# Performance work log

Measured on AMD Instinct MI355X. Metric: run time of the kernel, lower is better.

The kernel has to match this reference:

```python
import math
import jax, jax.numpy as jnp
import numpy as np

# Module config (init_kwargs)
GRID = (11, 16, 24)          # (T, H, W) latent grid, T odd so T-1 == 2*(T//2)
POOL = 128                   # pool_size / block size
SPARSITY = 0.9
TXT_LEN = 384                # txt_len, txt_first=False
HEADS, HDIM = 8, 128
FFL = GRID[1] * GRID[2]      # first_frame_len = H*W = 384
SEQ = GRID[0] * FFL + TXT_LEN  # 4608 tokens, 36 blocks of 128


def _rearr(t):
    # rearrange_with_remaining, h%8==0 and w%8==0 path.
    # t: [b, (f h w), n, d] with f = T-1 frames (first frame excluded)
    b, s, n, d = t.shape
    T, H, W = GRID
    fn, hn, wn = T // 2, H // 8, W // 8
    x = t.transpose(0, 2, 1, 3).reshape(b * n, fn, 2, hn, 8, wn, 8, d)
    # 'b (fn fb)(hn hb)(wn wb) d -> b (fn hn wn fb hb wb) d'
    x = x.transpose(0, 1, 3, 5, 2, 4, 6, 7).reshape(b * n, s, d)
    return x.reshape(b, n, s, d).transpose(0, 2, 1, 3)


def _inv_rearr(t):
    b, s, n, d = t.shape
    T, H, W = GRID
    fn, hn, wn = T // 2, H // 8, W // 8
    x = t.transpose(0, 2, 1, 3).reshape(b * n, fn, hn, wn, 2, 8, 8, d)
    x = x.transpose(0, 1, 4, 2, 5, 3, 6, 7).reshape(b * n, s, d)
    return x.reshape(b, n, s, d).transpose(0, 2, 1, 3)


def _avgpool(t):
    # seq divisible by POOL -> mean over each block (tail branch unused)
    b, s, n, d = t.shape
    return t.reshape(b, s // POOL, POOL, n, d).mean(axis=2)


def _forward(q, k, v):
    b, s, n, d = q.shape
    scale = jnp.asarray(d, q.dtype) ** -0.5
    # do_tensor_rearrange_pooling on concatenated qkv (txt_first=False)
    qkv = jnp.concatenate([q, k, v], axis=0)
    f_part = qkv[:, :FFL]
    i_part = qkv[:, FFL:s - TXT_LEN]
    t_part = qkv[:, s - TXT_LEN:]
    qkv2 = jnp.concatenate([_rearr(i_part), f_part, t_part], axis=1)
    pool = _avgpool(qkv2)
    q2, k2, v2 = jnp.split(qkv2, 3, axis=0)
    qp, kp, _ = jnp.split(pool, 3, axis=0)
    # pooled block scores + softmax
    ps = jax.nn.softmax(jnp.einsum('blnd,bsnd->bnls', qp, kp) * scale, axis=-1)
    nb = s // POOL
    keep = math.ceil(nb * (1.0 - SPARSITY))
    thr = jax.lax.top_k(ps, keep)[0][..., -1:]
    mask = ps >= thr                              # [B, n, nb, nb] bool
    prot = (FFL + TXT_LEN + POOL - 1) // POOL
    mask = mask.at[:, :, -prot:, :].set(True)
    mask = mask.at[:, :, :, -prot:].set(True)
    bm = mask[0]                                  # [n, nb, nb] per-head block mask (batch 0, as kernel uses)
    tok = jnp.repeat(jnp.repeat(bm, POOL, axis=1), POOL, axis=2)  # [n, S, S]
    # block-sparse attention == masked dense attention over selected kv blocks
    scores = jnp.einsum('bqnd,bknd->bnqk', q2, k2) * scale
    scores = jnp.where(tok[None], scores, jnp.asarray(-1e30, scores.dtype))
    p = jax.nn.softmax(scores, axis=-1)
    x = jnp.einsum('bnqk,bknd->bqnd', p, v2)
    # do_tensor_inv_rearrange (txt_first=False: concat(f, i, t))
    si = s - TXT_LEN - FFL
    xi = _inv_rearr(x[:, :si])
    xf = x[:, si:si + FFL]
    xt = x[:, si + FFL:]
    return jnp.concatenate([xf, xi, xt], axis=1)


def setup_inputs() -> dict:
    key = jax.random.key(0)
    kq, kk, kv = jax.random.split(key, 3)
    q = jax.random.normal(kq, (1, SEQ, HEADS, HDIM), dtype=jnp.float32)
    k = jax.random.normal(kk, (1, SEQ, HEADS, HDIM), dtype=jnp.float32)
    v = jax.random.normal(kv, (1, SEQ, HEADS, HDIM), dtype=jnp.float32)
    t_b_idx = jnp.arange(2, dtype=jnp.int64 if jax.config.jax_enable_x64 else jnp.int32)
    return {'q': q, 'k': k, 'v': v, 't_b_idx': t_b_idx}


def reference(q, k, v, t_b_idx):
    # t_idx = t_b_idx[0] = 0, skip_timesteps = 0 -> sparse branch (static)
    return _forward(q, k, v)
```

## Files before the change

kernel.cpp:

```cpp
#include <hip/hip_runtime.h>


typedef __attribute__((ext_vector_type(8))) _Float16 half8;
typedef __attribute__((ext_vector_type(4))) _Float16 half4;
typedef __attribute__((ext_vector_type(4))) float float4v;

#define KROW 136
#define VROW 72
#define PPROW 40

__device__ __forceinline__ int orig_pos(int j) {
    if (j >= 3840) return (j < 4224) ? (j - 3840) : j;
    int blk = j >> 7;
    int r   = j & 127;
    int f   = blk / 6;
    int rem = blk - f * 6;
    int b2  = rem / 3;
    int e   = rem - b2 * 3;
    int a   = r >> 6;
    int c   = (r >> 3) & 7;
    int g   = r & 7;
    return 384 + (f * 2 + a) * 384 + (b2 * 8 + c) * 24 + e * 8 + g;
}

__global__ __launch_bounds__(256) void prep_kernel(const float* __restrict__ q,
                                                   const float* __restrict__ k,
                                                   const float* __restrict__ v,
                                                   short* __restrict__ Kc,
                                                   unsigned* __restrict__ Vt32,
                                                   float* __restrict__ qp,
                                                   float* __restrict__ kp) {
    __shared__ short Vs[64 * KROW];
    __shared__ float Rs[8 * 128];
    int bx  = blockIdx.x;
    int tid = threadIdx.x;

    if (bx < 576) {
        int sub = bx & 1;
        int kb  = (bx >> 1) % 36;
        int h   = bx / 72;

        int lr = tid >> 3;
        int ld = (tid & 7) << 2;
#pragma unroll
        for (int pass = 0; pass < 2; ++pass) {
            int lt  = pass * 32 + lr;
            int tok = sub * 64 + lt;
            int op  = orig_pos(kb * 128 + tok);
            const float* kr = k + ((size_t)op * 8 + h) * 128;
            const float* vr = v + ((size_t)op * 8 + h) * 128;
            short* ko = Kc + ((size_t)(h * 36 + kb) * 128 + tok) * KROW;
#pragma unroll
            for (int j = 0; j < 4; ++j) {
                int d = ld + j * 32;
                float4v xk = *reinterpret_cast<const float4v*>(kr + d);
                float4v xv = *reinterpret_cast<const float4v*>(vr + d);
                half4 hk, hv;
#pragma unroll
                for (int i = 0; i < 4; ++i) { hk[i] = (_Float16)xk[i]; hv[i] = (_Float16)xv[i]; }
                *reinterpret_cast<half4*>(ko + d) = hk;
                *reinterpret_cast<half4*>(&Vs[lt * KROW + d]) = hv;
            }
        }
        __syncthreads();

        {
            const unsigned short* Vsu = (const unsigned short*)Vs;
            unsigned* vo = Vt32 + (size_t)((h * 36 + kb) * 2 + sub) * 128 * (VROW / 2);
#pragma unroll
            for (int it = 0; it < 16; ++it) {
                int i   = it * 256 + tid;
                int tw  = i & 31;
                int dim = i >> 5;
                unsigned lo = Vsu[(2 * tw) * KROW + dim];
                unsigned hi = Vsu[(2 * tw + 1) * KROW + dim];
                vo[dim * (VROW / 2) + tw] = (hi << 16) | lo;
            }
        }
    } else {
        int bx2 = bx - 576;
        int sub = bx2 & 1;
        int kb  = (bx2 >> 1) % 36;
        int h   = bx2 / 72;

        const float* arr = sub ? q : k;
        int dq = (tid & 31) << 2;
        int g  = tid >> 5;
        float4v acc = {0.f, 0.f, 0.f, 0.f};
#pragma unroll
        for (int it = 0; it < 16; ++it) {
            int t  = g + it * 8;
            int op = orig_pos(kb * 128 + t);
            float4v x = *reinterpret_cast<const float4v*>(arr + ((size_t)op * 8 + h) * 128 + dq);
            acc[0] += x[0]; acc[1] += x[1]; acc[2] += x[2]; acc[3] += x[3];
        }
#pragma unroll
        for (int i = 0; i < 4; ++i) Rs[g * 128 + dq + i] = acc[i];
        __syncthreads();

        if (tid < 128) {
            float s = 0.f;
#pragma unroll
            for (int g2 = 0; g2 < 8; ++g2) s += Rs[g2 * 128 + tid];
            float* outp = sub ? qp : kp;
            outp[(h * 36 + kb) * 128 + tid] = s * (1.f / 128.f);
        }
    }
}

__global__ __launch_bounds__(256, 3) void flash_kernel(const float* __restrict__ q,
                                                       const short* __restrict__ Kc,
                                                       const short* __restrict__ Vt,
                                                       const float* __restrict__ qp,
                                                       const float* __restrict__ kp,
                                                       float* __restrict__ out,
                                                       float* __restrict__ pO,
                                                       float* __restrict__ pL) {
    __shared__ __align__(16) short Ph[4 * 32 * PPROW];
    __shared__ __align__(16) float Red[2][32 * 132];
    __shared__ int Ls[40];
    __shared__ float Lf[64];

    int t = blockIdx.x;
    int h, qb, half, nkb = 0, kbase = 0, pidx = -1;
    if (t < 288) {
        h = t & 7;
        int rest = t >> 3;
        int qbh = rest / 6, r2 = rest % 6;
        half = r2 / 3;
        int chunk = r2 % 3;
        qb = 30 + qbh; nkb = 12; kbase = chunk * 12; pidx = t;
    } else {
        int t2 = t - 288;
        h = t2 & 7;
        int rest = t2 >> 3;
        qb = rest >> 1; half = rest & 1;
    }

    int tid = threadIdx.x, wave = tid >> 6, lane = tid & 63;
    int m16 = lane & 15, quad = lane >> 4;
    int rh = wave & 1, th = wave >> 1;

    constexpr float kScale = 0.08838834764831845f * 1.4426950408889634f;

    half8 aq[2][4];
#pragma unroll
    for (int rg = 0; rg < 2; ++rg) {
        int qrow_frag = qb * 128 + half * 64 + rh * 32 + rg * 16 + m16;
        const float* qrp = q + ((size_t)orig_pos(qrow_frag) * 8 + h) * 128;
#pragma unroll
        for (int kc = 0; kc < 4; ++kc) {
            float4v x0 = *reinterpret_cast<const float4v*>(qrp + kc * 32 + quad * 8);
            float4v x1 = *reinterpret_cast<const float4v*>(qrp + kc * 32 + quad * 8 + 4);
#pragma unroll
            for (int j = 0; j < 4; ++j) {
                aq[rg][kc][j]     = (_Float16)(x0[j] * kScale);
                aq[rg][kc][4 + j] = (_Float16)(x1[j] * kScale);
            }
        }
    }

    if (pidx < 0 && wave == 0) {
        float s = -1e30f;
        if (lane < 36) {
            const float4v* qv = (const float4v*)(qp + (h * 36 + qb) * 128);
            const float4v* kv = (const float4v*)(kp + (h * 36 + lane) * 128);
            float acc = 0.f;
            for (int i = 0; i < 32; ++i) {
                float4v a = qv[i], b = kv[i];
                acc += a[0] * b[0] + a[1] * b[1] + a[2] * b[2] + a[3] * b[3];
            }
            s = acc;
        }
        float tmp = s;
        float thr = 0.f;
        for (int i = 0; i < 4; ++i) {
            float mx = tmp;
            for (int off = 1; off < 64; off <<= 1) mx = fmaxf(mx, __shfl_xor(mx, off));
            thr = mx;
            unsigned long long bal = __ballot(tmp == mx);
            int low = __ffsll(bal) - 1;
            if (lane == low) tmp = -3e38f;
        }
        bool keep = (lane < 36) && ((s >= thr) || (lane >= 30));
        unsigned long long mk = __ballot(keep);
        if (lane == 0) Ls[0] = __popcll(mk);
        if (keep) {
            int pos = __popcll(mk & ((1ull << lane) - 1ull));
            Ls[1 + pos] = lane;
        }
    }
    __syncthreads();
    if (pidx < 0) nkb = Ls[0];

    float l_r[2][4];
    float4v o[2][8];
#pragma unroll
    for (int rg = 0; rg < 2; ++rg) {
#pragma unroll
        for (int r = 0; r < 4; ++r) l_r[rg][r] = 0.f;
#pragma unroll
        for (int dt = 0; dt < 8; ++dt) { o[rg][dt][0] = 0.f; o[rg][dt][1] = 0.f; o[rg][dt][2] = 0.f; o[rg][dt][3] = 0.f; }
    }

    short* Phw = Ph + wave * (32 * PPROW);

    int kfo = (th * 32 + m16) * KROW + quad * 8;
    int vfo = m16 * VROW + th * 32 + quad * 8;

    int ntile = nkb * 2;
    for (int it = 0; it < ntile; ++it) {
        int kb  = (pidx >= 0) ? (kbase + (it >> 1)) : Ls[1 + (it >> 1)];
        int sub = it & 1;
        const short* gK = Kc + ((size_t)((h * 36 + kb) * 128) + sub * 64) * KROW;
        const short* gV = Vt + (size_t)((h * 36 + kb) * 2 + sub) * 128 * VROW;

        float4v sacc[2][2];
#pragma unroll
        for (int rg = 0; rg < 2; ++rg)
#pragma unroll
            for (int nt = 0; nt < 2; ++nt) { sacc[rg][nt][0] = 0.f; sacc[rg][nt][1] = 0.f; sacc[rg][nt][2] = 0.f; sacc[rg][nt][3] = 0.f; }
#pragma unroll
        for (int nt = 0; nt < 2; ++nt)
#pragma unroll
            for (int kc = 0; kc < 4; ++kc) {
                half8 bk = *reinterpret_cast<const half8*>(gK + kfo + nt * (16 * KROW) + kc * 32);
                sacc[0][nt] = __builtin_amdgcn_mfma_f32_16x16x32_f16(aq[0][kc], bk, sacc[0][nt], 0, 0, 0);
                sacc[1][nt] = __builtin_amdgcn_mfma_f32_16x16x32_f16(aq[1][kc], bk, sacc[1][nt], 0, 0, 0);
            }

#pragma unroll
        for (int rg = 0; rg < 2; ++rg)
#pragma unroll
            for (int r = 0; r < 4; ++r) {
                float p0 = exp2f(sacc[rg][0][r]);
                float p1 = exp2f(sacc[rg][1][r]);
                sacc[rg][0][r] = p0; sacc[rg][1][r] = p1;
                l_r[rg][r] += p0 + p1;
            }

#pragma unroll
        for (int rg = 0; rg < 2; ++rg)
#pragma unroll
            for (int nt = 0; nt < 2; ++nt)
#pragma unroll
                for (int r = 0; r < 4; ++r) {
                    union { _Float16 hf; short s; } cv;
                    cv.hf = (_Float16)sacc[rg][nt][r];
                    Phw[(rg * 16 + quad * 4 + r) * PPROW + nt * 16 + m16] = cv.s;
                }
        half8 ap[2];
#pragma unroll
        for (int rg = 0; rg < 2; ++rg)
            ap[rg] = *reinterpret_cast<const half8*>(&Phw[(rg * 16 + m16) * PPROW + quad * 8]);

#pragma unroll
        for (int dt = 0; dt < 8; ++dt) {
            half8 bv = *reinterpret_cast<const half8*>(gV + vfo + dt * (16 * VROW));
            o[0][dt] = __builtin_amdgcn_mfma_f32_16x16x32_f16(ap[0], bv, o[0][dt], 0, 0, 0);
            o[1][dt] = __builtin_amdgcn_mfma_f32_16x16x32_f16(ap[1], bv, o[1][dt], 0, 0, 0);
        }
    }

#pragma unroll
    for (int rg = 0; rg < 2; ++rg)
#pragma unroll
        for (int r = 0; r < 4; ++r)
            for (int sh = 1; sh < 16; sh <<= 1) l_r[rg][r] += __shfl_xor(l_r[rg][r], sh);

    __syncthreads();
    {
        float* red = &Red[rh][0];
        if (th == 1) {
#pragma unroll
            for (int rg = 0; rg < 2; ++rg) {
#pragma unroll
                for (int dt = 0; dt < 8; ++dt)
#pragma unroll
                    for (int r = 0; r < 4; ++r)
                        red[(rg * 16 + quad * 4 + r) * 132 + dt * 16 + m16] = o[rg][dt][r];
                if (m16 == 0)
#pragma unroll
                    for (int r = 0; r < 4; ++r)
                        Lf[rh * 32 + rg * 16 + quad * 4 + r] = l_r[rg][r];
            }
        }
        __syncthreads();
        if (th == 0) {
#pragma unroll
            for (int rg = 0; rg < 2; ++rg)
#pragma unroll
                for (int dt = 0; dt < 8; ++dt)
#pragma unroll
                    for (int r = 0; r < 4; ++r)
                        o[rg][dt][r] += red[(rg * 16 + quad * 4 + r) * 132 + dt * 16 + m16];

            if (pidx >= 0) {
                float* po = pO + (size_t)pidx * 8192;
#pragma unroll
                for (int rg = 0; rg < 2; ++rg)
#pragma unroll
                    for (int r = 0; r < 4; ++r) {
                        int row = rh * 32 + rg * 16 + quad * 4 + r;
                        float lt2 = l_r[rg][r] + Lf[row];
#pragma unroll
                        for (int dt = 0; dt < 8; ++dt)
                            po[row * 128 + dt * 16 + m16] = o[rg][dt][r];
                        if (m16 == 0) pL[pidx * 64 + row] = lt2;
                    }
            } else {
#pragma unroll
                for (int rg = 0; rg < 2; ++rg)
#pragma unroll
                    for (int r = 0; r < 4; ++r) {
                        int row = rh * 32 + rg * 16 + quad * 4 + r;
                        int qrow = qb * 128 + half * 64 + row;
                        size_t base = ((size_t)orig_pos(qrow) * 8 + h) * 128;
                        float inv = 1.f / (l_r[rg][r] + Lf[row]);
#pragma unroll
                        for (int dt = 0; dt < 8; ++dt)
                            out[base + dt * 16 + m16] = o[rg][dt][r] * inv;
                    }
            }
        }
    }
}

__global__ void combine_kernel(const float* __restrict__ pO, const float* __restrict__ pL,
                               float* __restrict__ out) {
    int gb = blockIdx.x;
    int g  = gb >> 3;
    int rg = gb & 7;
    int h    = g / 12;
    int rem  = g % 12;
    int qbh  = rem >> 1;
    int half = rem & 1;
    int qb   = 30 + qbh;
    int base_t = (qbh * 6 + half * 3) * 8 + h;

    int tid = threadIdx.x;
    int d   = tid & 127;
    int r0  = tid >> 7;
#pragma unroll
    for (int itr = 0; itr < 4; ++itr) {
        int row = rg * 8 + r0 + itr * 2;
        float l = pL[(base_t + 0) * 64 + row] + pL[(base_t + 8) * 64 + row] + pL[(base_t + 16) * 64 + row];
        float acc = pO[(size_t)(base_t + 0) * 8192 + row * 128 + d]
                  + pO[(size_t)(base_t + 8) * 8192 + row * 128 + d]
                  + pO[(size_t)(base_t + 16) * 8192 + row * 128 + d];
        int qrow = qb * 128 + half * 64 + row;
        out[((size_t)orig_pos(qrow) * 8 + h) * 128 + d] = acc / l;
    }
}

extern "C" void kernel_launch(void* const* d_in, const int* in_sizes, int n_in,
                              void* d_out, int out_size, void* d_ws, size_t ws_size,
                              hipStream_t stream) {
    const float* q = (const float*)d_in[0];
    const float* k = (const float*)d_in[1];
    const float* v = (const float*)d_in[2];
    float* out = (float*)d_out;

    char* w = (char*)d_ws;
    short* Kc  = (short*)(w);
    short* Vt  = (short*)(w + 10027008);
    float* qp  = (float*)(w + 20643840);
    float* kp  = (float*)(w + 20791296);
    float* pL  = (float*)(w + 20938752);
    float* pO  = (float*)(w + 21012480);

    prep_kernel<<<dim3(1152), dim3(256), 0, stream>>>(q, k, v, Kc, (unsigned*)Vt, qp, kp);
    flash_kernel<<<dim3(768), dim3(256), 0, stream>>>(q, Kc, Vt, qp, kp, out, pO, pL);
    combine_kernel<<<dim3(768), dim3(256), 0, stream>>>(pO, pL, out);
}
```

Baseline: 175.1 us.

## Stage Q fragments in LDS and software-prefetch next K tile into registers

Moves the scaled fp16 Q fragments out of registers into a shared-memory buffer that is aliased with the reduction scratch, freeing VGPRs. The freed registers hold a double-buffered prefetch: the next tile's K fragments load during the current PV stage, and V fragments are issued before the softmax. The goal is to hide global-load latency behind the MFMA work. In exchange, each QK step now re-reads Q from LDS, and the extra live K and V registers may still push up register pressure at the 3-blocks-per-SM launch bound.

```diff
diff --git a/kernel.cpp b/kernel.cpp
--- a/kernel.cpp
+++ b/kernel.cpp
@@ -8,6 +8,7 @@
 #define KROW 136
 #define VROW 72
 #define PPROW 40
+#define QROW 136
 
 __device__ __forceinline__ int orig_pos(int j) {
     if (j >= 3840) return (j < 4224) ? (j - 3840) : j;
@@ -117,9 +118,11 @@
                                                        float* __restrict__ pO,
                                                        float* __restrict__ pL) {
     __shared__ __align__(16) short Ph[4 * 32 * PPROW];
-    __shared__ __align__(16) float Red[2][32 * 132];
+    __shared__ __align__(16) char  UB[34816];
     __shared__ int Ls[40];
     __shared__ float Lf[64];
+    short* Qlds = (short*)UB;
+    float* RedF = (float*)UB;
 
     int t = blockIdx.x;
     int h, qb, half, nkb = 0, kbase = 0, pidx = -1;
@@ -143,20 +146,22 @@
 
     constexpr float kScale = 0.08838834764831845f * 1.4426950408889634f;
 
-    half8 aq[2][4];
 #pragma unroll
     for (int rg = 0; rg < 2; ++rg) {
         int qrow_frag = qb * 128 + half * 64 + rh * 32 + rg * 16 + m16;
         const float* qrp = q + ((size_t)orig_pos(qrow_frag) * 8 + h) * 128;
+        short* qdst = Qlds + ((wave * 2 + rg) * 16 + m16) * QROW + quad * 8;
 #pragma unroll
         for (int kc = 0; kc < 4; ++kc) {
             float4v x0 = *reinterpret_cast<const float4v*>(qrp + kc * 32 + quad * 8);
             float4v x1 = *reinterpret_cast<const float4v*>(qrp + kc * 32 + quad * 8 + 4);
+            half8 a;
 #pragma unroll
             for (int j = 0; j < 4; ++j) {
-                aq[rg][kc][j]     = (_Float16)(x0[j] * kScale);
-                aq[rg][kc][4 + j] = (_Float16)(x1[j] * kScale);
-            }
+                a[j]     = (_Float16)(x0[j] * kScale);
+                a[4 + j] = (_Float16)(x1[j] * kScale);
+            }
+            *reinterpret_cast<half8*>(qdst + kc * 32) = a;
         }
     }
 
@@ -204,15 +209,27 @@
     }
 
     short* Phw = Ph + wave * (32 * PPROW);
+    const short* Qw = Qlds + (wave * 2) * 16 * QROW + m16 * QROW + quad * 8;
 
     int kfo = (th * 32 + m16) * KROW + quad * 8;
     int vfo = m16 * VROW + th * 32 + quad * 8;
 
     int ntile = nkb * 2;
+    half8 bk[8], bv[8];
+
+    {
+        int kb0 = (pidx >= 0) ? kbase : Ls[1];
+        const short* gK0 = Kc + ((size_t)((h * 36 + kb0) * 128)) * KROW;
+#pragma unroll
+        for (int nt = 0; nt < 2; ++nt)
+#pragma unroll
+            for (int kc = 0; kc < 4; ++kc)
+                bk[nt * 4 + kc] = *reinterpret_cast<const half8*>(gK0 + kfo + nt * (16 * KROW) + kc * 32);
+    }
+
     for (int it = 0; it < ntile; ++it) {
         int kb  = (pidx >= 0) ? (kbase + (it >> 1)) : Ls[1 + (it >> 1)];
         int sub = it & 1;
-        const short* gK = Kc + ((size_t)((h * 36 + kb) * 128) + sub * 64) * KROW;
         const short* gV = Vt + (size_t)((h * 36 + kb) * 2 + sub) * 128 * VROW;
 
         float4v sacc[2][2];
@@ -221,13 +238,18 @@
 #pragma unroll
             for (int nt = 0; nt < 2; ++nt) { sacc[rg][nt][0] = 0.f; sacc[rg][nt][1] = 0.f; sacc[rg][nt][2] = 0.f; sacc[rg][nt][3] = 0.f; }
 #pragma unroll
-        for (int nt = 0; nt < 2; ++nt)
-#pragma unroll
-            for (int kc = 0; kc < 4; ++kc) {
-                half8 bk = *reinterpret_cast<const half8*>(gK + kfo + nt * (16 * KROW) + kc * 32);
-                sacc[0][nt] = __builtin_amdgcn_mfma_f32_16x16x32_f16(aq[0][kc], bk, sacc[0][nt], 0, 0, 0);
-                sacc[1][nt] = __builtin_amdgcn_mfma_f32_16x16x32_f16(aq[1][kc], bk, sacc[1][nt], 0, 0, 0);
-            }
+        for (int kc = 0; kc < 4; ++kc) {
+            half8 a0 = *reinterpret_cast<const half8*>(Qw + kc * 32);
+            half8 a1 = *reinterpret_cast<const half8*>(Qw + 16 * QROW + kc * 32);
+            sacc[0][0] = __builtin_amdgcn_mfma_f32_16x16x32_f16(a0, bk[kc],     sacc[0][0], 0, 0, 0);
+            sacc[1][0] = __builtin_amdgcn_mfma_f32_16x16x32_f16(a1, bk[kc],     sacc[1][0], 0, 0, 0);
+            sacc[0][1] = __builtin_amdgcn_mfma_f32_16x16x32_f16(a0, bk[4 + kc], sacc[0][1], 0, 0, 0);
+            sacc[1][1] = __builtin_amdgcn_mfma_f32_16x16x32_f16(a1, bk[4 + kc], sacc[1][1], 0, 0, 0);
+        }
+
+#pragma unroll
+        for (int dt = 0; dt < 8; ++dt)
+            bv[dt] = *reinterpret_cast<const half8*>(gV + vfo + dt * (16 * VROW));
 
 #pragma unroll
         for (int rg = 0; rg < 2; ++rg)
@@ -254,11 +276,21 @@
         for (int rg = 0; rg < 2; ++rg)
             ap[rg] = *reinterpret_cast<const half8*>(&Phw[(rg * 16 + m16) * PPROW + quad * 8]);
 
+        if (it + 1 < ntile) {
+            int kb2  = (pidx >= 0) ? (kbase + ((it + 1) >> 1)) : Ls[1 + ((it + 1) >> 1)];
+            int sub2 = (it + 1) & 1;
+            const short* gK2 = Kc + ((size_t)((h * 36 + kb2) * 128) + sub2 * 64) * KROW;
+#pragma unroll
+            for (int nt = 0; nt < 2; ++nt)
+#pragma unroll
+                for (int kc = 0; kc < 4; ++kc)
+                    bk[nt * 4 + kc] = *reinterpret_cast<const half8*>(gK2 + kfo + nt * (16 * KROW) + kc * 32);
+        }
+
 #pragma unroll
         for (int dt = 0; dt < 8; ++dt) {
-            half8 bv = *reinterpret_cast<const half8*>(gV + vfo + dt * (16 * VROW));
-            o[0][dt] = __builtin_amdgcn_mfma_f32_16x16x32_f16(ap[0], bv, o[0][dt], 0, 0, 0);
-            o[1][dt] = __builtin_amdgcn_mfma_f32_16x16x32_f16(ap[1], bv, o[1][dt], 0, 0, 0);
+            o[0][dt] = __builtin_amdgcn_mfma_f32_16x16x32_f16(ap[0], bv[dt], o[0][dt], 0, 0, 0);
+            o[1][dt] = __builtin_amdgcn_mfma_f32_16x16x32_f16(ap[1], bv[dt], o[1][dt], 0, 0, 0);
         }
     }
 
@@ -270,7 +302,7 @@
 
     __syncthreads();
     {
-        float* red = &Red[rh][0];
+        float* red = RedF + rh * (32 * 132);
         if (th == 1) {
 #pragma unroll
             for (int rg = 0; rg < 2; ++rg) {
```

Result: slower. 269.5 us (+53.9%).
